# Kernel optimization log

Hardware: AMD Instinct MI355X
Metric: run time of the kernel (lower is better)

## Reference

```python
import jax, jax.numpy as jnp
import numpy as np

INO, INN, HID = 128, 128, 64

def _xavier(key, shape):
    fan_in, fan_out = shape[0], shape[1]
    limit = float(np.sqrt(6.0 / (fan_in + fan_out)))
    return jax.random.uniform(key, shape, jnp.float32, -limit, limit)

def setup_inputs() -> dict:
    key = jax.random.key(0)
    k1, k2, k3, k4 = jax.random.split(key, 4)
    xo = jax.random.normal(k1, (512, INO), jnp.float32)
    xn = jax.random.normal(k2, (2048, INN), jnp.float32)
    W1 = _xavier(k3, (INO + INN, HID))  # Linear(ino+inn, hidden).weight.T
    b1 = jnp.zeros((HID,), jnp.float32)
    W2 = _xavier(k4, (HID, 1))          # Linear(hidden, 1).weight.T
    b2 = jnp.zeros((1,), jnp.float32)
    return {"xo": xo, "xn": xn, "W1": W1, "b1": b1, "W2": W2, "b2": b2}

def reference(xo, xn, W1, b1, W2, b2):
    # cat([xo_expanded, xn_expanded]) @ W1 == xo @ W1[:ino] + xn @ W1[ino:]
    ino = xo.shape[1]
    pre = xo @ W1[:ino]                      # [B, H]
    pre_n = xn @ W1[ino:]                    # [N, H]
    h = jax.nn.leaky_relu(pre[:, None, :] + pre_n[None, :, :] + b1, 0.2)  # [B, N, H]
    scores = jnp.einsum('bnh,h->bn', h, W2[:, 0]) + b2[0]                  # [B, N]
    att = jax.nn.softmax(scores, axis=1)                                   # [B, N]
    return att @ xn                                                        # [B, inn]
```

## Files before the change

### kernel.cpp

```cpp
#include <hip/hip_runtime.h>
#include <math.h>

#define INO 128
#define INN 128
#define HID 64
#define NB  512
#define NN  2048
#define TB  4
#define NCH 8
#define NPC (NN / NCH)

__global__ __launch_bounds__(256) void pre_kernel(
    const float* __restrict__ xo, const float* __restrict__ xn,
    const float* __restrict__ W1, const float* __restrict__ b1,
    float* __restrict__ pre)
{
    int t = blockIdx.x * blockDim.x + threadIdx.x;
    int row = t >> 6;
    int h = t & 63;
    if (row >= NB + NN) return;
    const float* x;
    const float* w;
    float a0, a1 = 0.f, a2 = 0.f, a3 = 0.f;
    if (row < NB) { x = xo + row * INO;        w = W1;             a0 = b1[h]; }
    else          { x = xn + (row - NB) * INN; w = W1 + INO * HID; a0 = 0.f;  }
    const float4* x4 = (const float4*)x;
#pragma unroll
    for (int k4 = 0; k4 < INO / 4; ++k4) {
        float4 xv = x4[k4];
        int kb = k4 * 4;
        a0 = fmaf(xv.x, w[(kb + 0) * HID + h], a0);
        a1 = fmaf(xv.y, w[(kb + 1) * HID + h], a1);
        a2 = fmaf(xv.z, w[(kb + 2) * HID + h], a2);
        a3 = fmaf(xv.w, w[(kb + 3) * HID + h], a3);
    }
    pre[row * HID + h] = (a0 + a1) + (a2 + a3);
}

__global__ __launch_bounds__(256) void score_pv_kernel(
    const float* __restrict__ pre, const float* __restrict__ xn,
    const float* __restrict__ W2,
    float* __restrict__ ssum, float* __restrict__ part)
{
    const int bt = blockIdx.x >> 3;
    const int ch = blockIdx.x & 7;
    const int b0 = bt * TB;
    const int n0 = ch * NPC;
    const int tid = threadIdx.x;
    const int lane = tid & 63, wid = tid >> 6;

    __shared__ float4 s_p4[NPC];
    __shared__ float  s_red[4][TB];
    __shared__ float4 s_part4[8][TB][INN / 4];

    const float* pre_n = pre + NB * HID;
    const float* po = pre + b0 * HID;

    float acc[TB] = {0.f, 0.f, 0.f, 0.f};
    const float4* pn = (const float4*)(pre_n + (n0 + tid) * HID);
#pragma unroll 4
    for (int j = 0; j < HID / 4; ++j) {
        float4 v = pn[j];
#pragma unroll
        for (int hh = 0; hh < 4; ++hh) {
            const int h = 4 * j + hh;
            const float w = W2[h];
            const float e = (&v.x)[hh];
#pragma unroll
            for (int b = 0; b < TB; ++b) {
                float t = po[b * HID + h] + e;
                acc[b] = fmaf(fmaxf(t, 0.2f * t), w, acc[b]);
            }
        }
    }

    float p[TB];
#pragma unroll
    for (int b = 0; b < TB; ++b) {
        p[b] = __expf(acc[b]);
        float s = p[b];
#pragma unroll
        for (int o = 32; o > 0; o >>= 1) s += __shfl_xor(s, o, 64);
        if (lane == 0) s_red[wid][b] = s;
    }
    s_p4[tid] = make_float4(p[0], p[1], p[2], p[3]);
    __syncthreads();
    if (tid < TB) {
        float sm = s_red[0][tid] + s_red[1][tid] +
                   s_red[2][tid] + s_red[3][tid];
        ssum[ch * NB + b0 + tid] = sm;
    }

    const int c4 = tid & 31;
    const int g  = tid >> 5;
    float4 f[TB];
#pragma unroll
    for (int b = 0; b < TB; ++b) f[b] = make_float4(0.f, 0.f, 0.f, 0.f);
    const float* xp = xn + (size_t)(n0 + g * 32) * INN + c4 * 4;
#pragma unroll 8
    for (int k = 0; k < 32; ++k) {
        float4 xv = *(const float4*)(xp + (size_t)k * INN);
        float4 pv = s_p4[g * 32 + k];
        f[0].x = fmaf(pv.x, xv.x, f[0].x);
        f[0].y = fmaf(pv.x, xv.y, f[0].y);
        f[0].z = fmaf(pv.x, xv.z, f[0].z);
        f[0].w = fmaf(pv.x, xv.w, f[0].w);
        f[1].x = fmaf(pv.y, xv.x, f[1].x);
        f[1].y = fmaf(pv.y, xv.y, f[1].y);
        f[1].z = fmaf(pv.y, xv.z, f[1].z);
        f[1].w = fmaf(pv.y, xv.w, f[1].w);
        f[2].x = fmaf(pv.z, xv.x, f[2].x);
        f[2].y = fmaf(pv.z, xv.y, f[2].y);
        f[2].z = fmaf(pv.z, xv.z, f[2].z);
        f[2].w = fmaf(pv.z, xv.w, f[2].w);
        f[3].x = fmaf(pv.w, xv.x, f[3].x);
        f[3].y = fmaf(pv.w, xv.y, f[3].y);
        f[3].z = fmaf(pv.w, xv.z, f[3].z);
        f[3].w = fmaf(pv.w, xv.w, f[3].w);
    }
#pragma unroll
    for (int b = 0; b < TB; ++b) s_part4[g][b][c4] = f[b];
    __syncthreads();
    if (tid < TB * (INN / 4)) {
        int b = tid >> 5, cc = tid & 31;
        float4 s = make_float4(0.f, 0.f, 0.f, 0.f);
#pragma unroll
        for (int gg = 0; gg < 8; ++gg) {
            float4 v = s_part4[gg][b][cc];
            s.x += v.x; s.y += v.y; s.z += v.z; s.w += v.w;
        }
        *(float4*)&part[(size_t)(ch * NB + b0 + b) * INN + cc * 4] = s;
    }
}

__global__ __launch_bounds__(256) void combine_kernel(
    const float* __restrict__ ssum, const float* __restrict__ part,
    float* __restrict__ out)
{
    int idx = blockIdx.x * 256 + threadIdx.x;
    int b = idx >> 7, c = idx & 127;
    float den = 0.f, num = 0.f;
#pragma unroll
    for (int ch = 0; ch < NCH; ++ch) {
        den += ssum[ch * NB + b];
        num += part[(size_t)(ch * NB + b) * INN + c];
    }
    out[idx] = num / den;
}

extern "C" void kernel_launch(void* const* d_in, const int* in_sizes, int n_in,
                              void* d_out, int out_size, void* d_ws, size_t ws_size,
                              hipStream_t stream) {
    const float* xo = (const float*)d_in[0];
    const float* xn = (const float*)d_in[1];
    const float* W1 = (const float*)d_in[2];
    const float* b1 = (const float*)d_in[3];
    const float* W2 = (const float*)d_in[4];
    float* out = (float*)d_out;

    float* pre  = (float*)d_ws;
    float* ssum = pre + (NB + NN) * HID;
    float* part = ssum + NCH * NB;

    const int total = (NB + NN) * HID;
    pre_kernel<<<(total + 255) / 256, 256, 0, stream>>>(xo, xn, W1, b1, pre);
    score_pv_kernel<<<(NB / TB) * NCH, 256, 0, stream>>>(pre, xn, W2, ssum, part);
    combine_kernel<<<(NB * INN) / 256, 256, 0, stream>>>(ssum, part, out);
}
```

Before: 86.29 us.

## Split N into 16 chunks and map thread halves to batch row pairs

Doubles the number of node chunks so the score kernel launches twice as many blocks, each covering 128 nodes. The 256 threads now split into two halves, each scoring 128 nodes for two batch rows, which halves the per-thread exp and accumulator work. The probabilities are stored as a [node][batch] shared array and read as float4 in the weighted-sum stage. This raises occupancy and parallelism, at the cost of loading each pre_n row twice and doubling the partial sums the combine kernel must read. The combine kernel still loops over NCH, which now includes the extra chunks.

```diff
diff --git a/kernel.cpp b/kernel.cpp
--- a/kernel.cpp
+++ b/kernel.cpp
@@ -7,8 +7,9 @@
 #define NB  512
 #define NN  2048
 #define TB  4
-#define NCH 8
+#define NCH 16
 #define NPC (NN / NCH)
+#define NBT (NB / TB)
 
 __global__ __launch_bounds__(256) void pre_kernel(
     const float* __restrict__ xo, const float* __restrict__ xn,
@@ -42,22 +43,24 @@
     const float* __restrict__ W2,
     float* __restrict__ ssum, float* __restrict__ part)
 {
-    const int bt = blockIdx.x >> 3;
-    const int ch = blockIdx.x & 7;
+    const int bt = blockIdx.x >> 4;
+    const int ch = blockIdx.x & 15;
     const int b0 = bt * TB;
     const int n0 = ch * NPC;
     const int tid = threadIdx.x;
     const int lane = tid & 63, wid = tid >> 6;
 
-    __shared__ float4 s_p4[NPC];
-    __shared__ float  s_red[4][TB];
+    __shared__ float  s_p[NPC][TB];
+    __shared__ float  s_red[4][2];
     __shared__ float4 s_part4[8][TB][INN / 4];
 
     const float* pre_n = pre + NB * HID;
-    const float* po = pre + b0 * HID;
+    const int nl = tid & 127;
+    const int bp = __builtin_amdgcn_readfirstlane(tid >> 7);
+    const float* po = pre + (b0 + bp * 2) * HID;
 
-    float acc[TB] = {0.f, 0.f, 0.f, 0.f};
-    const float4* pn = (const float4*)(pre_n + (n0 + tid) * HID);
+    float acc[2] = {0.f, 0.f};
+    const float4* pn = (const float4*)(pre_n + (n0 + nl) * HID);
 #pragma unroll 4
     for (int j = 0; j < HID / 4; ++j) {
         float4 v = pn[j];
@@ -67,28 +70,28 @@
             const float w = W2[h];
             const float e = (&v.x)[hh];
 #pragma unroll
-            for (int b = 0; b < TB; ++b) {
-                float t = po[b * HID + h] + e;
-                acc[b] = fmaf(fmaxf(t, 0.2f * t), w, acc[b]);
+            for (int bb = 0; bb < 2; ++bb) {
+                float t = po[bb * HID + h] + e;
+                acc[bb] = fmaf(fmaxf(t, 0.2f * t), w, acc[bb]);
             }
         }
     }
 
-    float p[TB];
+    float p0 = __expf(acc[0]);
+    float p1 = __expf(acc[1]);
+    s_p[nl][bp * 2 + 0] = p0;
+    s_p[nl][bp * 2 + 1] = p1;
+    float s0 = p0, s1 = p1;
 #pragma unroll
-    for (int b = 0; b < TB; ++b) {
-        p[b] = __expf(acc[b]);
-        float s = p[b];
-#pragma unroll
-        for (int o = 32; o > 0; o >>= 1) s += __shfl_xor(s, o, 64);
-        if (lane == 0) s_red[wid][b] = s;
+    for (int o = 32; o > 0; o >>= 1) {
+        s0 += __shfl_xor(s0, o, 64);
+        s1 += __shfl_xor(s1, o, 64);
     }
-    s_p4[tid] = make_float4(p[0], p[1], p[2], p[3]);
+    if (lane == 0) { s_red[wid][0] = s0; s_red[wid][1] = s1; }
     __syncthreads();
     if (tid < TB) {
-        float sm = s_red[0][tid] + s_red[1][tid] +
-                   s_red[2][tid] + s_red[3][tid];
-        ssum[ch * NB + b0 + tid] = sm;
+        int bb = tid & 1, w0 = (tid >> 1) * 2;
+        ssum[ch * NB + b0 + tid] = s_red[w0][bb] + s_red[w0 + 1][bb];
     }
 
     const int c4 = tid & 31;
@@ -96,11 +99,11 @@
     float4 f[TB];
 #pragma unroll
     for (int b = 0; b < TB; ++b) f[b] = make_float4(0.f, 0.f, 0.f, 0.f);
-    const float* xp = xn + (size_t)(n0 + g * 32) * INN + c4 * 4;
+    const float* xp = xn + (size_t)(n0 + g * 16) * INN + c4 * 4;
 #pragma unroll 8
-    for (int k = 0; k < 32; ++k) {
+    for (int k = 0; k < 16; ++k) {
         float4 xv = *(const float4*)(xp + (size_t)k * INN);
-        float4 pv = s_p4[g * 32 + k];
+        float4 pv = *(const float4*)&s_p[g * 16 + k][0];
         f[0].x = fmaf(pv.x, xv.x, f[0].x);
         f[0].y = fmaf(pv.x, xv.y, f[0].y);
         f[0].z = fmaf(pv.x, xv.z, f[0].z);
@@ -164,6 +167,6 @@
 
     const int total = (NB + NN) * HID;
     pre_kernel<<<(total + 255) / 256, 256, 0, stream>>>(xo, xn, W1, b1, pre);
-    score_pv_kernel<<<(NB / TB) * NCH, 256, 0, stream>>>(pre, xn, W2, ssum, part);
+    score_pv_kernel<<<NBT * NCH, 256, 0, stream>>>(pre, xn, W2, ssum, part);
     combine_kernel<<<(NB * INN) / 256, 256, 0, stream>>>(ssum, part, out);
 }
```

New measurement: 96.00 us. +11.3%, slower.
